# Kernel optimization log

Measured on AMD Instinct MI355X. Metric: run time of the kernel, lower is better.

Reference implementation:

```python
import jax, jax.numpy as jnp
import numpy as np

B, L, C, P, H, DK, MRD = 16, 1024, 512, 64, 8, 64, 7
STD = 0.02


def _layernorm(x, g, b):
    mu = x.mean(-1, keepdims=True)
    var = ((x - mu) ** 2).mean(-1, keepdims=True)
    return (x - mu) / jnp.sqrt(var + 1e-5) * g + b


def _rel_pos_table(L, m):
    i = jnp.arange(L)
    d = jnp.abs(i[:, None] - i[None, :]).astype(jnp.float32)
    d = jnp.where(d > m, m + jnp.log2(jnp.maximum(d - m, 1.0)), d)
    return jnp.clip(d, 0, 2 * m).astype(jnp.int32)  # (L, L) in [0, 2m]


def setup_inputs() -> dict:
    key = jax.random.key(0)
    ks = jax.random.split(key, 16)
    inp = {
        'qx': jax.random.normal(ks[0], (B, L, C), jnp.float32),
        'kx': jax.random.normal(ks[1], (B, L, C), jnp.float32),
        'vx': jax.random.normal(ks[2], (B, L, C), jnp.float32),
        'maskPAD': jnp.ones((B, L, L), jnp.int32),
        'Wp': jax.random.normal(ks[3], (C, P)) * STD,
        'bp': jnp.zeros((P,)),
        'WQ': jax.random.normal(ks[4], (C, H * DK)) * STD,
        'bQ': jnp.zeros((H * DK,)),
        'WK': jax.random.normal(ks[5], (C, H * DK)) * STD,
        'bK': jnp.zeros((H * DK,)),
        'WV': jax.random.normal(ks[6], (C, H * DK)) * STD,
        'bV': jnp.zeros((H * DK,)),
        'WO': jax.random.normal(ks[7], (H * DK, C)) * STD,
        'bO': jnp.zeros((C,)),
        'embK': jax.random.normal(ks[8], (2 * MRD + 1, H)) * STD,
        'embB': jax.random.normal(ks[9], (2 * MRD + 1, H)) * STD,
        'ln1_g': jnp.ones((C,)), 'ln1_b': jnp.zeros((C,)),
        'ln2_g': jnp.ones((C,)), 'ln2_b': jnp.zeros((C,)),
        'W1': jax.random.normal(ks[10], (C, 4 * C)) * STD,
        'b1': jnp.zeros((4 * C,)),
        'W2': jax.random.normal(ks[11], (4 * C, C)) * STD,
        'b2': jnp.zeros((C,)),
    }
    return inp


def reference(qx, kx, vx, maskPAD, Wp, bp, WQ, bQ, WK, bK, WV, bV, WO, bO,
              embK, embB, ln1_g, ln1_b, ln2_g, ln2_b, W1, b1, W2, b2):
    B_, L_, C_ = qx.shape
    P_ = Wp.shape[1]
    H_ = embK.shape[1]
    DK_ = WV.shape[1] // H_
    m = (embK.shape[0] - 1) // 2

    # pseudo-token attention pooling
    pScore = vx @ Wp + bp                                   # (B, L, P)
    pad = (maskPAD[:, 0] == 0)                              # (B, L)
    pScore = jnp.where(pad[:, :, None], -2.0 ** 15, pScore)
    pAlpha = jax.nn.softmax(pScore, axis=1)                 # softmax over L
    kxp = jnp.einsum('blp,blc->bpc', pAlpha, kx)            # (B, P, C)
    vxp = jnp.einsum('blp,blc->bpc', pAlpha, vx)
    pA = jax.lax.stop_gradient(pAlpha)                      # .detach()

    # multi-head attention vs pseudo tokens
    q = (qx @ WQ + bQ).reshape(B_, L_, H_, DK_).transpose(0, 2, 1, 3)   # (B,H,L,dk)
    k = (kxp @ WK + bK).reshape(B_, P_, H_, DK_).transpose(0, 2, 1, 3)  # (B,H,P,dk)
    v = (vxp @ WV + bV).reshape(B_, P_, H_, DK_).transpose(0, 2, 1, 3)
    scores = jnp.einsum('bhld,bhpd->bhlp', q, k) / np.sqrt(DK_).astype(np.float32)

    # relative position multiplicative/additive bias, pooled through pA
    tab = _rel_pos_table(L_, m)                             # (L, L)
    Krel = embK[tab].transpose(2, 0, 1)                     # (H, L, L)
    brel = embB[tab].transpose(2, 0, 1)
    Kb = jnp.einsum('hlm,bmp->bhlp', Krel, pA)
    bb = jnp.einsum('hlm,bmp->bhlp', brel, pA)
    scores = scores * Kb + bb

    alpha = jax.nn.softmax(scores, axis=3)
    z = jnp.einsum('bhlp,bhpd->bhld', alpha, v)
    z = z.transpose(0, 2, 1, 3).reshape(B_, L_, H_ * DK_)
    z = z @ WO + bO

    # FFN block (residuals against vx, post-LN)
    z1 = _layernorm(vx + z, ln1_g, ln1_b)
    ffn = jax.nn.gelu(z1 @ W1 + b1, approximate=False) @ W2 + b2
    x = _layernorm(z1 + ffn, ln2_g, ln2_b)
    return x
```

## Files before the change

### kernel.cpp

```cpp
#include <hip/hip_runtime.h>
#include <hip/hip_bf16.h>

#define BI   16
#define LSEQ 1024
#define CDIM 512
#define PDIM 64
#define HH   8
#define DKK  64

typedef __hip_bfloat16 bf16;
typedef unsigned short u16;
typedef __attribute__((ext_vector_type(8))) short bf16x8;
typedef __attribute__((ext_vector_type(4))) float f32x4;

__constant__ int c_dlo[15] = {0,1,2,3,4,5,6,7, 9,11,15,23,39, 71,135};
__constant__ int c_dhi[15] = {0,1,2,3,4,5,6,8,10,14,22,38,70,134,1023};

__device__ __forceinline__ float b2f(u16 u) {
    union { unsigned int i; float f; } c; c.i = ((unsigned int)u) << 16; return c.f;
}
__device__ __forceinline__ u16 f2bu(float v) {
    bf16 h = __float2bfloat16(v);
    return *(u16*)&h;
}
__device__ __forceinline__ float ldDyn(const void* p, size_t i, int f) {
    return f ? ((const float*)p)[i] : b2f(((const u16*)p)[i]);
}
__device__ __forceinline__ void ld4Dyn(const void* p, size_t i, int f, float* o) {
    if (f) { float4 v = *(const float4*)((const float*)p + i);
             o[0]=v.x; o[1]=v.y; o[2]=v.z; o[3]=v.w; }
    else   { ushort4 u = *(const ushort4*)((const u16*)p + i);
             o[0]=b2f(u.x); o[1]=b2f(u.y); o[2]=b2f(u.z); o[3]=b2f(u.w); }
}

__device__ __forceinline__ void gll16(const u16* g, u16* l) {
    __builtin_amdgcn_global_load_lds(
        (const __attribute__((address_space(1))) unsigned int*)g,
        (__attribute__((address_space(3))) unsigned int*)l,
        16, 0, 0);
}

__device__ __forceinline__ float wsum(float v) {
    #pragma unroll
    for (int o = 32; o; o >>= 1) v += __shfl_xor(v, o, 64);
    return v;
}
__device__ __forceinline__ float wmax(float v) {
    #pragma unroll
    for (int o = 32; o; o >>= 1) v = fmaxf(v, __shfl_xor(v, o, 64));
    return v;
}

__device__ __forceinline__ float gelu_f(float v) {
    float x  = v * 0.70710678118654752f;
    float ax = fabsf(x);
    float t  = __builtin_amdgcn_rcpf(1.0f + 0.3275911f * ax);
    float p  = t * (0.254829592f + t * (-0.284496736f + t * (1.421413741f +
               t * (-1.453152027f + t * 1.061405429f))));
    float e  = __expf(-ax * ax);
    float er = 1.0f - p * e;
    er = (x < 0.0f) ? -er : er;
    return 0.5f * v * (1.0f + er);
}

__global__ void k_detect(const unsigned int* __restrict__ qw, int* __restrict__ flag) {
    __shared__ int cnt;
    if (threadIdx.x == 0) cnt = 0;
    __syncthreads();
    int local = 0;
    for (int i = threadIdx.x; i < 4096; i += 256) {
        float fv = b2f((u16)(qw[i] & 0xFFFFu));
        float af = fabsf(fv);
        if (fv == 0.0f || (af >= 0.0009765625f && af <= 32.0f)) local++;
    }
    atomicAdd(&cnt, local);
    __syncthreads();
    if (threadIdx.x == 0) flag[0] = (cnt >= 2048) ? 0 : 1;
}

__global__ __launch_bounds__(256) void k_cvt2(
    const void* __restrict__ s0, u16* __restrict__ d0,
    const void* __restrict__ s1, u16* __restrict__ d1,
    const int* __restrict__ flag, int n)
{
    const int fA = flag[0];
    const void* src = blockIdx.y ? s1 : s0;
    u16* dst = blockIdx.y ? d1 : d0;
    int i = (blockIdx.x * 256 + threadIdx.x) * 4;
    if (i >= n) return;
    float t[4]; ld4Dyn(src, i, fA, t);
    ushort4 o; o.x = f2bu(t[0]); o.y = f2bu(t[1]); o.z = f2bu(t[2]); o.w = f2bu(t[3]);
    *(ushort4*)(dst + i) = o;
}

__device__ __forceinline__ void transp_core(
    const void* W, u16* WT, int fd, int Kd, int Nd, int bx, int by)
{
    __shared__ u16 t[32][33];
    const int tx = threadIdx.x & 31, ty = threadIdx.x >> 5;
    #pragma unroll
    for (int r = 0; r < 32; r += 8) {
        int k = by * 32 + ty + r, n = bx * 32 + tx;
        t[ty + r][tx] = f2bu(ldDyn(W, (size_t)k * Nd + n, fd));
    }
    __syncthreads();
    #pragma unroll
    for (int r = 0; r < 32; r += 8) {
        int n = bx * 32 + ty + r, k = by * 32 + tx;
        WT[(size_t)n * Kd + k] = t[tx][ty + r];
    }
}

__global__ __launch_bounds__(256) void k_transp(
    const void* __restrict__ W, u16* __restrict__ WT, const int* __restrict__ flag,
    int Kd, int Nd)
{
    transp_core(W, WT, flag[0], Kd, Nd, blockIdx.x, blockIdx.y);
}

__global__ __launch_bounds__(256) void k_transp4(
    const void* __restrict__ W0, u16* __restrict__ T0,
    const void* __restrict__ W1, u16* __restrict__ T1,
    const void* __restrict__ W2, u16* __restrict__ T2,
    const void* __restrict__ W3, u16* __restrict__ T3,
    const int* __restrict__ flag)
{
    const void* W; u16* T;
    switch (blockIdx.z) {
        case 0: W = W0; T = T0; break;
        case 1: W = W1; T = T1; break;
        case 2: W = W2; T = T2; break;
        default: W = W3; T = T3; break;
    }
    transp_core(W, T, flag[0], 512, 512, blockIdx.x, blockIdx.y);
}

__global__ __launch_bounds__(256) void k_transpcv(
    const void* __restrict__ kx, const u16* __restrict__ vxb,
    u16* __restrict__ kxT, u16* __restrict__ vxT, const int* __restrict__ flag)
{
    const int t = blockIdx.z >> 4;
    const int b = blockIdx.z & 15;
    const int l0 = blockIdx.x * 64, c0 = blockIdx.y * 32;
    __shared__ u16 s[32][72];
    const int tid = threadIdx.x;
    if (t == 0) {
        const int fd = flag[0];
        #pragma unroll
        for (int p = 0; p < 2; ++p) {
            int l = (tid >> 3) + p * 32, c4 = (tid & 7) * 4;
            float v[4];
            ld4Dyn(kx, ((size_t)b * LSEQ + l0 + l) * CDIM + c0 + c4, fd, v);
            #pragma unroll
            for (int k = 0; k < 4; ++k) s[c4 + k][l] = f2bu(v[k]);
        }
    } else {
        #pragma unroll
        for (int p = 0; p < 2; ++p) {
            int l = (tid >> 3) + p * 32, c4 = (tid & 7) * 4;
            ushort4 u = *(const ushort4*)&vxb[((size_t)b * LSEQ + l0 + l) * CDIM + c0 + c4];
            s[c4 + 0][l] = u.x; s[c4 + 1][l] = u.y;
            s[c4 + 2][l] = u.z; s[c4 + 3][l] = u.w;
        }
    }
    __syncthreads();
    u16* dst = t ? vxT : kxT;
    #pragma unroll
    for (int p = 0; p < 2; ++p) {
        int c = (tid >> 4) + p * 16, l4 = (tid & 15) * 4;
        *(ushort4*)&dst[((size_t)b * CDIM + c0 + c) * LSEQ + l0 + l4] =
            *(const ushort4*)&s[c][l4];
    }
}

__device__ __forceinline__ void gemm_core(
    u16 (*As)[32], u16 (*Bs)[32],
    const u16* A, const u16* BT, const void* bias, const u16* res, void* Cc, int fd,
    int K, int lda, int ldbt, int ldc, size_t bOff, int mode, int outBf, int perm,
    int m0, int n0)
{
    const int tid = threadIdx.x;
    const int wave = tid >> 6, lane = tid & 63;
    const int q = lane >> 4, l16 = lane & 15;
    const int wm = (wave >> 2) * 64, wn = (wave & 3) * 64;
    const int srow = lane >> 2;
    const int scol = ((lane & 3) ^ ((lane >> 3) & 3)) * 8;
    const int rchk = (l16 >> 1) & 3;
    const int nt = K >> 5;

    f32x4 acc[4][4];
    #pragma unroll
    for (int i = 0; i < 4; ++i)
        #pragma unroll
        for (int j = 0; j < 4; ++j) acc[i][j] = (f32x4){0.f, 0.f, 0.f, 0.f};

    auto stage = [&](int t, int buf) {
        gll16(A + (size_t)(m0 + wave * 16 + srow) * lda + t * 32 + scol,
              &As[buf * 128 + wave * 16][0]);
        #pragma unroll
        for (int pass = 0; pass < 2; ++pass)
            gll16(BT + (size_t)(n0 + pass * 128 + wave * 16 + srow) * ldbt + t * 32 + scol,
                  &Bs[buf * 256 + pass * 128 + wave * 16][0]);
    };

    stage(0, 0);

    for (int t = 0; t < nt; ++t) {
        if (t + 1 < nt) {
            stage(t + 1, (t + 1) & 1);
            asm volatile("s_waitcnt vmcnt(3)" ::: "memory");
        } else {
            asm volatile("s_waitcnt vmcnt(0)" ::: "memory");
        }
        __builtin_amdgcn_sched_barrier(0);
        __builtin_amdgcn_s_barrier();

        const int ca = (t & 1) * 128, cbB = (t & 1) * 256;
        bf16x8 af[4], bfr[4];
        #pragma unroll
        for (int i = 0; i < 4; ++i)
            af[i] = *(const bf16x8*)&As[ca + wm + i * 16 + l16][(q ^ rchk) * 8];
        #pragma unroll
        for (int j = 0; j < 4; ++j)
            bfr[j] = *(const bf16x8*)&Bs[cbB + wn + j * 16 + l16][(q ^ rchk) * 8];
        #pragma unroll
        for (int i = 0; i < 4; ++i)
            #pragma unroll
            for (int j = 0; j < 4; ++j)
                acc[i][j] = __builtin_amdgcn_mfma_f32_16x16x32_bf16(af[i], bfr[j], acc[i][j], 0, 0, 0);

        if (t + 1 < nt) {
            asm volatile("s_waitcnt lgkmcnt(0)" ::: "memory");
            __builtin_amdgcn_sched_barrier(0);
            __builtin_amdgcn_s_barrier();
        }
    }

    float bv[4];
    #pragma unroll
    for (int j = 0; j < 4; ++j)
        bv[j] = ldDyn(bias, bOff + (size_t)(n0 + wn + j * 16 + l16), fd);

    #pragma unroll
    for (int i = 0; i < 4; ++i) {
        int row = m0 + wm + i * 16 + q * 4;
        #pragma unroll
        for (int j = 0; j < 4; ++j) {
            int col = n0 + wn + j * 16 + l16;
            #pragma unroll
            for (int r = 0; r < 4; ++r) {
                float v = acc[i][j][r] + bv[j];
                int m = row + r;
                if (mode == 2) {
                    v += b2f(res[(size_t)m * ldc + col]);
                    if (outBf) ((u16*)Cc)[(size_t)m * ldc + col] = f2bu(v);
                    else       ((float*)Cc)[(size_t)m * ldc + col] = v;
                } else {
                    if (mode == 1) v = gelu_f(v);
                    size_t idx = perm ? (size_t)((m >> 6) << 15) + ((size_t)col << 6) + (m & 63)
                                      : (size_t)m * ldc + col;
                    if (outBf) ((u16*)Cc)[idx] = f2bu(v);
                    else       ((float*)Cc)[idx] = v;
                }
            }
        }
    }
}

__global__ __launch_bounds__(512) void gemm_mfma(
    const u16* __restrict__ A, const u16* __restrict__ BT, const void* __restrict__ bias,
    const u16* __restrict__ res, void* __restrict__ Cc, const int* __restrict__ flag,
    int K, int lda, int ldbt, int ldc, size_t bOff, int mode, int outBf, int perm)
{
    __shared__ u16 As[256][32];
    __shared__ u16 Bs[512][32];
    const int lin = blockIdx.y * gridDim.x + blockIdx.x;
    const int chunk = (gridDim.x * gridDim.y) >> 3;
    const int wg = (lin & 7) * chunk + (lin >> 3);
    const int bx = wg % gridDim.x, by = wg / gridDim.x;
    gemm_core(As, Bs, A, BT, bias, res, Cc, flag[0], K, lda, ldbt, ldc, bOff,
              mode, outBf, perm, by * 128, bx * 256);
}

__global__ __launch_bounds__(512) void gemm_kv(
    const u16* __restrict__ A0, const u16* __restrict__ A1,
    const u16* __restrict__ BT0, const u16* __restrict__ BT1,
    const void* __restrict__ b0, const void* __restrict__ b1,
    void* __restrict__ C0, void* __restrict__ C1, const int* __restrict__ flag)
{
    __shared__ u16 As[256][32];
    __shared__ u16 Bs[512][32];
    const int z = blockIdx.z;
    gemm_core(As, Bs, z ? A1 : A0, z ? BT1 : BT0, z ? b1 : b0, nullptr,
              z ? C1 : C0, flag[0],
              CDIM, CDIM, CDIM, CDIM, 0, 0, 1, z ? 1 : 0,
              blockIdx.y * 128, blockIdx.x * 256);
}

__global__ __launch_bounds__(256) void gemm_pool(
    const u16* __restrict__ pAT, const u16* __restrict__ kxT,
    const u16* __restrict__ vxT, u16* __restrict__ kvxb)
{
    __shared__ u16 As[128][32];
    __shared__ u16 Bs[256][32];
    const int b = blockIdx.y;
    const int n0 = blockIdx.x * 128;
    const u16* Ag = pAT + (size_t)b * (PDIM * LSEQ);
    const u16* Bg = (blockIdx.z ? vxT : kxT) + (size_t)b * (CDIM * LSEQ);
    u16* Cg = kvxb + (size_t)blockIdx.z * 524288 + (size_t)b * (PDIM * CDIM);

    const int tid = threadIdx.x;
    const int wave = tid >> 6, lane = tid & 63;
    const int q = lane >> 4, l16 = lane & 15;
    const int wm = (wave >> 1) * 32, wn = (wave & 1) * 64;
    const int srow = lane >> 2, scol = (lane & 3) * 8;

    f32x4 acc[2][4];
    #pragma unroll
    for (int i = 0; i < 2; ++i)
        #pragma unroll
        for (int j = 0; j < 4; ++j) acc[i][j] = (f32x4){0.f, 0.f, 0.f, 0.f};

    gll16(Ag + (size_t)(wave * 16 + srow) * LSEQ + scol, &As[wave * 16][0]);
    #pragma unroll
    for (int pass = 0; pass < 2; ++pass)
        gll16(Bg + (size_t)(n0 + wave * 32 + pass * 16 + srow) * LSEQ + scol,
              &Bs[wave * 32 + pass * 16][0]);
    __syncthreads();

    int cur = 0;
    for (int k0 = 0; k0 < LSEQ; k0 += 32) {
        if (k0 + 32 < LSEQ) {
            const int na = (cur ^ 1) * 64, nb = (cur ^ 1) * 128;
            gll16(Ag + (size_t)(wave * 16 + srow) * LSEQ + (k0 + 32) + scol,
                  &As[na + wave * 16][0]);
            #pragma unroll
            for (int pass = 0; pass < 2; ++pass)
                gll16(Bg + (size_t)(n0 + wave * 32 + pass * 16 + srow) * LSEQ + (k0 + 32) + scol,
                      &Bs[nb + wave * 32 + pass * 16][0]);
        }
        const int ca = cur * 64, cb = cur * 128;
        bf16x8 af[2], bfr[4];
        #pragma unroll
        for (int i = 0; i < 2; ++i) af[i] = *(const bf16x8*)&As[ca + wm + i * 16 + l16][q * 8];
        #pragma unroll
        for (int j = 0; j < 4; ++j) bfr[j] = *(const bf16x8*)&Bs[cb + wn + j * 16 + l16][q * 8];
        #pragma unroll
        for (int i = 0; i < 2; ++i)
            #pragma unroll
            for (int j = 0; j < 4; ++j)
                acc[i][j] = __builtin_amdgcn_mfma_f32_16x16x32_bf16(af[i], bfr[j], acc[i][j], 0, 0, 0);
        __syncthreads();
        cur ^= 1;
    }

    #pragma unroll
    for (int i = 0; i < 2; ++i) {
        int row = wm + i * 16 + q * 4;
        #pragma unroll
        for (int j = 0; j < 4; ++j) {
            int col = n0 + wn + j * 16 + l16;
            #pragma unroll
            for (int r = 0; r < 4; ++r)
                Cg[(size_t)(row + r) * CDIM + col] = f2bu(acc[i][j][r]);
        }
    }
}

__global__ __launch_bounds__(256) void gemm_mfma64(
    const u16* __restrict__ A, const u16* __restrict__ BT, const void* __restrict__ bias,
    float* __restrict__ Cc, const int* __restrict__ flag,
    int K, int lda, int ldbt)
{
    const int fd = flag[0];
    __shared__ u16 As[256][32];
    __shared__ u16 Bs[128][32];
    const int m0 = blockIdx.y * 128;
    const int tid = threadIdx.x;
    const int wave = tid >> 6, lane = tid & 63;
    const int q = lane >> 4, l16 = lane & 15;
    const int wm = wave * 32;
    const int srow = wave * 16 + (lane >> 2);
    const int scol = (lane & 3) * 8;

    f32x4 acc[2][4];
    #pragma unroll
    for (int i = 0; i < 2; ++i)
        #pragma unroll
        for (int j = 0; j < 4; ++j) acc[i][j] = (f32x4){0.f, 0.f, 0.f, 0.f};

    #pragma unroll
    for (int pass = 0; pass < 2; ++pass) {
        int row = pass * 64 + srow;
        gll16(A + (size_t)(m0 + row) * lda + scol, &As[pass * 64 + wave * 16][0]);
    }
    gll16(BT + (size_t)srow * ldbt + scol, &Bs[wave * 16][0]);
    __syncthreads();

    int cur = 0;
    for (int k0 = 0; k0 < K; k0 += 32) {
        if (k0 + 32 < K) {
            const int na = (cur ^ 1) * 128, nb = (cur ^ 1) * 64;
            #pragma unroll
            for (int pass = 0; pass < 2; ++pass) {
                int row = pass * 64 + srow;
                gll16(A + (size_t)(m0 + row) * lda + (k0 + 32) + scol,
                      &As[na + pass * 64 + wave * 16][0]);
            }
            gll16(BT + (size_t)srow * ldbt + (k0 + 32) + scol, &Bs[nb + wave * 16][0]);
        }
        const int ca = cur * 128, cb = cur * 64;
        bf16x8 af[2], bfr[4];
        #pragma unroll
        for (int i = 0; i < 2; ++i) af[i] = *(const bf16x8*)&As[ca + wm + i * 16 + l16][q * 8];
        #pragma unroll
        for (int j = 0; j < 4; ++j) bfr[j] = *(const bf16x8*)&Bs[cb + j * 16 + l16][q * 8];
        #pragma unroll
        for (int i = 0; i < 2; ++i)
            #pragma unroll
            for (int j = 0; j < 4; ++j)
                acc[i][j] = __builtin_amdgcn_mfma_f32_16x16x32_bf16(af[i], bfr[j], acc[i][j], 0, 0, 0);
        __syncthreads();
        cur ^= 1;
    }

    #pragma unroll
    for (int i = 0; i < 2; ++i) {
        int row = m0 + wm + i * 16 + q * 4;
        #pragma unroll
        for (int j = 0; j < 4; ++j) {
            int col = j * 16 + l16;
            #pragma unroll
            for (int r = 0; r < 4; ++r)
                Cc[(size_t)(row + r) * 64 + col] = acc[i][j][r] + ldDyn(bias, col, fd);
        }
    }
}

__global__ __launch_bounds__(256) void gemm_att(
    const u16* __restrict__ Abase, const u16* __restrict__ Bbase,
    void* __restrict__ outp, int mode)
{
    __shared__ u16 Aq[2][128][32];
    __shared__ u16 Bk[2][64][32];
    const int bh = blockIdx.y;
    const int b = bh >> 3, h = bh & 7;
    const int m0 = blockIdx.x * 128;
    const int tid = threadIdx.x;
    const int wave = tid >> 6, lane = tid & 63;
    const int q = lane >> 4, l16 = lane & 15;

    const u16* Ag; const u16* Bg; int lda, ldb;
    if (mode == 0) {
        Ag = Abase + ((size_t)b * LSEQ + m0) * CDIM + h * 64;  lda = CDIM;
        Bg = Bbase + (size_t)b * 32768 + h * 64;               ldb = CDIM;
    } else {
        Ag = Abase + ((size_t)bh * LSEQ + m0) * 64;            lda = 64;
        Bg = Bbase + (size_t)b * 32768 + (size_t)h * 64 * 64;  ldb = 64;
    }

    const int srow = lane >> 2;
    const int scol = (lane & 3) * 8;
    #pragma unroll
    for (int half = 0; half < 2; ++half) {
        #pragma unroll
        for (int pass = 0; pass < 2; ++pass) {
            int row = pass * 64 + wave * 16 + srow;
            gll16(Ag + (size_t)row * lda + half * 32 + scol,
                  &Aq[half][pass * 64 + wave * 16][0]);
        }
        gll16(Bg + (size_t)(wave * 16 + srow) * ldb + half * 32 + scol,
              &Bk[half][wave * 16][0]);
    }
    __syncthreads();

    f32x4 acc[2][4];
    #pragma unroll
    for (int i = 0; i < 2; ++i)
        #pragma unroll
        for (int j = 0; j < 4; ++j) acc[i][j] = (f32x4){0.f, 0.f, 0.f, 0.f};

    #pragma unroll
    for (int kk = 0; kk < 2; ++kk) {
        bf16x8 af[2], bfr[4];
        #pragma unroll
        for (int i = 0; i < 2; ++i)
            af[i] = *(const bf16x8*)&Aq[kk][wave * 32 + i * 16 + l16][q * 8];
        #pragma unroll
        for (int j = 0; j < 4; ++j)
            bfr[j] = *(const bf16x8*)&Bk[kk][j * 16 + l16][q * 8];
        #pragma unroll
        for (int i = 0; i < 2; ++i)
            #pragma unroll
            for (int j = 0; j < 4; ++j)
                acc[i][j] = __builtin_amdgcn_mfma_f32_16x16x32_bf16(af[i], bfr[j], acc[i][j], 0, 0, 0);
    }

    #pragma unroll
    for (int i = 0; i < 2; ++i) {
        int row = m0 + wave * 32 + i * 16 + q * 4;
        #pragma unroll
        for (int j = 0; j < 4; ++j) {
            int col = j * 16 + l16;
            #pragma unroll
            for (int r = 0; r < 4; ++r) {
                if (mode == 0) {
                    ((float*)outp)[((size_t)bh * LSEQ + row + r) * 64 + col] =
                        0.125f * acc[i][j][r];
                } else {
                    ((u16*)outp)[((size_t)b * LSEQ + row + r) * CDIM + h * 64 + col] =
                        f2bu(acc[i][j][r]);
                }
            }
        }
    }
}

__global__ __launch_bounds__(256) void k_softscan(
    const float* __restrict__ psc, const int* __restrict__ maskPAD,
    u16* __restrict__ pAT, float* __restrict__ cumT)
{
    const int b = blockIdx.x >> 6;
    const int p = blockIdx.x & 63;
    const int tid = threadIdx.x;
    __shared__ float s0[1024], s1[1024];
    __shared__ float redA[4], redB[4];

    float acc[4];
    #pragma unroll
    for (int r = 0; r < 4; ++r) {
        int m = tid + r * 256;
        float a = psc[((size_t)b * LSEQ + m) * PDIM + p];
        if (maskPAD[(size_t)b * LSEQ * LSEQ + m] == 0) a = -32768.0f;
        acc[r] = a;
    }
    float mx = fmaxf(fmaxf(acc[0], acc[1]), fmaxf(acc[2], acc[3]));
    mx = wmax(mx);
    if ((tid & 63) == 0) redA[tid >> 6] = mx;
    __syncthreads();
    mx = fmaxf(fmaxf(redA[0], redA[1]), fmaxf(redA[2], redA[3]));

    float e[4], ls = 0.f;
    #pragma unroll
    for (int r = 0; r < 4; ++r) { e[r] = expf(acc[r] - mx); ls += e[r]; }
    ls = wsum(ls);
    if ((tid & 63) == 0) redB[tid >> 6] = ls;
    __syncthreads();
    float inv = 1.0f / (redB[0] + redB[1] + redB[2] + redB[3]);

    #pragma unroll
    for (int r = 0; r < 4; ++r) {
        int m = tid + r * 256;
        float pa = e[r] * inv;
        pAT[((size_t)b * PDIM + p) * LSEQ + m] = f2bu(pa);
        s0[m] = pa;
    }
    __syncthreads();

    float* src = s0; float* dst = s1;
    for (int off = 1; off < 1024; off <<= 1) {
        #pragma unroll
        for (int r = 0; r < 4; ++r) {
            int i = tid + r * 256;
            float v = src[i];
            if (i >= off) v += src[i - off];
            dst[i] = v;
        }
        __syncthreads();
        float* t = src; src = dst; dst = t;
    }
    size_t cb = (size_t)b * (LSEQ + 1) * PDIM + p;
    if (tid == 0) cumT[cb] = 0.f;
    #pragma unroll
    for (int r = 0; r < 4; ++r) {
        int i = tid + r * 256;
        cumT[cb + (size_t)(i + 1) * PDIM] = src[i];
    }
}

__global__ __launch_bounds__(512) void k_sm(
    const float* __restrict__ raw, u16* __restrict__ alb,
    const float* __restrict__ cumT,
    const void* __restrict__ embK, const void* __restrict__ embB,
    const int* __restrict__ flag)
{
    const int fd = flag[0];
    const int b = blockIdx.x >> 10;
    const int l = blockIdx.x & 1023;
    const int tid = threadIdx.x;
    __shared__ float S[15][PDIM];
    __shared__ float eK[120], eB[120];

    if (tid < 120) { eK[tid] = ldDyn(embK, tid, fd); eB[tid] = ldDyn(embB, tid, fd); }

    const float* cb = cumT + (size_t)b * (LSEQ + 1) * PDIM;
    for (int idx = tid; idx < 960; idx += 512) {
        int t = idx >> 6, pp = idx & 63;
        float s;
        if (t == 0) {
            s = cb[(size_t)(l + 1) * 64 + pp] - cb[(size_t)l * 64 + pp];
        } else {
            s = 0.f;
            int hi = l - c_dlo[t];
            int lo = l - c_dhi[t]; if (lo < 0) lo = 0;
            if (hi >= lo) s += cb[(size_t)(hi + 1) * 64 + pp] - cb[(size_t)lo * 64 + pp];
            lo = l + c_dlo[t];
            hi = l + c_dhi[t]; if (hi > 1023) hi = 1023;
            if (lo <= hi) s += cb[(size_t)(hi + 1) * 64 + pp] - cb[(size_t)lo * 64 + pp];
        }
        S[t][pp] = s;
    }
    __syncthreads();

    const int h = tid >> 6, p = tid & 63;
    float kbm = 0.f, bbm = 0.f;
    #pragma unroll
    for (int t = 0; t < 15; ++t) {
        float sv = S[t][p];
        kbm += eK[t * 8 + h] * sv;
        bbm += eB[t * 8 + h] * sv;
    }
    size_t idx = (((size_t)b * 8 + h) * LSEQ + l) * 64 + p;
    float sc = raw[idx] * kbm + bbm;
    float mx = wmax(sc);
    float e  = expf(sc - mx);
    float ssum = wsum(e);
    alb[idx] = f2bu(e / ssum);
}

__global__ __launch_bounds__(512) void k_ln(
    const void* __restrict__ a, const u16* __restrict__ badd,
    const void* __restrict__ g, const void* __restrict__ be, const int* __restrict__ flag,
    void* __restrict__ out, float* __restrict__ out2, const void* __restrict__ bias2,
    int aKind, int outKind)
{
    const int fd = flag[0];
    const int fA = (aKind == 2) ? fd : aKind;
    const int fO = (outKind == 2) ? fd : outKind;
    const size_t row = blockIdx.x;
    const int c = threadIdx.x;
    float x = ldDyn(a, row * CDIM + c, fA);
    if (badd) x += b2f(badd[row * CDIM + c]);

    __shared__ float rA[8], rB[8];
    float s = wsum(x);
    if ((c & 63) == 0) rA[c >> 6] = s;
    __syncthreads();
    float tot = 0.f;
    #pragma unroll
    for (int w = 0; w < 8; ++w) tot += rA[w];
    float mu = tot * (1.0f / 512.0f);
    float dv = x - mu;
    float s2 = wsum(dv * dv);
    if ((c & 63) == 0) rB[c >> 6] = s2;
    __syncthreads();
    float v2 = 0.f;
    #pragma unroll
    for (int w = 0; w < 8; ++w) v2 += rB[w];
    float y = dv * rsqrtf(v2 * (1.0f / 512.0f) + 1e-5f) * ldDyn(g, c, fd) + ldDyn(be, c, fd);
    if (fO) ((float*)out)[row * CDIM + c] = y;
    else    ((u16*)out)[row * CDIM + c] = f2bu(y);
    if (out2) out2[row * CDIM + c] = y + ldDyn(bias2, c, fd);
}

extern "C" void kernel_launch(void* const* d_in, const int* in_sizes, int n_in,
                              void* d_out, int out_size, void* d_ws, size_t ws_size,
                              hipStream_t stream)
{
    (void)in_sizes; (void)n_in; (void)out_size; (void)ws_size;
    const void* qx   = d_in[0];
    const void* kx   = d_in[1];
    const void* vx   = d_in[2];
    const int*  mask = (const int*)d_in[3];
    const void* Wp   = d_in[4];
    const void* bp   = d_in[5];
    const void* WQ   = d_in[6];
    const void* bQ   = d_in[7];
    const void* WK   = d_in[8];
    const void* bK   = d_in[9];
    const void* WV   = d_in[10];
    const void* bV   = d_in[11];
    const void* WO   = d_in[12];
    const void* bO   = d_in[13];
    const void* embK = d_in[14];
    const void* embB = d_in[15];
    const void* l1g  = d_in[16];
    const void* l1b  = d_in[17];
    const void* l2g  = d_in[18];
    const void* l2b  = d_in[19];
    const void* W1   = d_in[20];
    const void* b1   = d_in[21];
    const void* W2   = d_in[22];
    const void* b2   = d_in[23];

    float* ws     = (float*)d_ws;
    int*   flag   = (int*)d_ws;
    u16*   outFb  = (u16*)(ws + 64);
    float* psc    = ws + 64;
    float* cumT   = ws + 1048640;
    u16*   pAT    = (u16*)(ws + 2098240);
    u16*   kbh    = (u16*)(ws + 2622528);
    u16*   vbT    = (u16*)(ws + 2884672);
    u16*   albuf  = (u16*)(ws + 3146816);
    u16*   kvxb   = (u16*)(ws + 7341120);
    u16*   qz     = (u16*)(ws + 8388672);
    u16*   hidden = (u16*)(ws + 12582976);
    u16*   qxb    = hidden;
    u16*   zo     = qxb;
    u16*   vxb    = (u16*)(ws + 16777280);
    u16*   kxT    = (u16*)(ws + 20971584);
    u16*   vxT    = (u16*)(ws + 25165888);
    float* rawbuf = ws + 20971584;
    u16*   WqT    = (u16*)(ws + 29360192);
    u16*   WkT    = (u16*)(ws + 29491264);
    u16*   WvT    = (u16*)(ws + 29622336);
    u16*   WoT    = (u16*)(ws + 29753408);
    u16*   W1T    = (u16*)(ws + 29884480);
    u16*   W2T    = (u16*)(ws + 30408768);
    u16*   WpT    = (u16*)(ws + 30933056);

    const int MROW = BI * LSEQ;

    k_detect<<<dim3(1), dim3(256), 0, stream>>>((const unsigned int*)qx, flag);
    k_cvt2<<<dim3(MROW * CDIM / 1024, 2), dim3(256), 0, stream>>>(
        qx, qxb, vx, vxb, flag, MROW * CDIM);
    k_transp4<<<dim3(16, 16, 4), dim3(256), 0, stream>>>(
        WQ, WqT, WK, WkT, WV, WvT, WO, WoT, flag);
    k_transp<<<dim3(2, 16),  dim3(256), 0, stream>>>(Wp, WpT, flag, 512, 64);
    k_transp<<<dim3(64, 16), dim3(256), 0, stream>>>(W1, W1T, flag, 512, 2048);
    k_transp<<<dim3(16, 64), dim3(256), 0, stream>>>(W2, W2T, flag, 2048, 512);
    k_transpcv<<<dim3(16, 16, 32), dim3(256), 0, stream>>>(kx, vxb, kxT, vxT, flag);

    gemm_mfma64<<<dim3(1, MROW / 128), dim3(256), 0, stream>>>(
        vxb, WpT, bp, psc, flag, CDIM, CDIM, CDIM);
    k_softscan<<<dim3(BI * PDIM), dim3(256), 0, stream>>>(psc, mask, pAT, cumT);
    gemm_pool<<<dim3(4, 16, 2), dim3(256), 0, stream>>>(pAT, kxT, vxT, kvxb);
    gemm_mfma<<<dim3(2, MROW / 128), dim3(512), 0, stream>>>(
        qxb, WqT, bQ, nullptr, qz, flag, CDIM, CDIM, CDIM, CDIM, 0, 0, 1, 0);
    gemm_kv<<<dim3(2, 8, 2), dim3(512), 0, stream>>>(
        kvxb, kvxb + 524288, WkT, WvT, bK, bV, kbh, vbT, flag);
    gemm_att<<<dim3(8, BI * HH), dim3(256), 0, stream>>>(qz, kbh, rawbuf, 0);
    k_sm<<<dim3(BI * LSEQ), dim3(512), 0, stream>>>(
        rawbuf, albuf, cumT, embK, embB, flag);
    gemm_att<<<dim3(8, BI * HH), dim3(256), 0, stream>>>(albuf, vbT, qz, 1);
    gemm_mfma<<<dim3(2, MROW / 128), dim3(512), 0, stream>>>(
        qz, WoT, bO, nullptr, zo, flag, CDIM, CDIM, CDIM, CDIM, 0, 0, 1, 0);
    k_ln<<<dim3(MROW), dim3(512), 0, stream>>>(
        vx, zo, l1g, l1b, flag, qz, nullptr, nullptr, 2, 0);
    gemm_mfma<<<dim3(8, MROW / 128), dim3(512), 0, stream>>>(
        qz, W1T, b1, nullptr, hidden, flag, CDIM, CDIM, CDIM, 2048, 0, 1, 1, 0);
    gemm_mfma<<<dim3(2, MROW / 128), dim3(512), 0, stream>>>(
        hidden, W2T, b2, qz, outFb, flag, 2048, 2048, 2048, CDIM, 0, 2, 1, 0);
    k_ln<<<dim3(MROW), dim3(512), 0, stream>>>(
        outFb, nullptr, l2g, l2b, flag, d_out, nullptr, nullptr, 0, 2);
}
```

Before: 613.2 us.

## Add four-stage LDS pipelined GEMM variant for narrow-N projections

Adds a gemm_core_deep path that uses four LDS buffers, issuing loads three tiles ahead with one barrier per iteration instead of two, and raises wave priority around the MFMA block. It is applied to the Q, O, K/V and W2 projection GEMMs (N=512), which launch only 256 workgroups and are likely latency-bound on global loads. LDS per block grows to 96KB, which can lower occupancy to one block per CU.

```diff
diff --git a/kernel.cpp b/kernel.cpp
--- a/kernel.cpp
+++ b/kernel.cpp
@@ -173,69 +173,11 @@
     }
 }
 
-__device__ __forceinline__ void gemm_core(
-    u16 (*As)[32], u16 (*Bs)[32],
-    const u16* A, const u16* BT, const void* bias, const u16* res, void* Cc, int fd,
-    int K, int lda, int ldbt, int ldc, size_t bOff, int mode, int outBf, int perm,
-    int m0, int n0)
-{
-    const int tid = threadIdx.x;
-    const int wave = tid >> 6, lane = tid & 63;
-    const int q = lane >> 4, l16 = lane & 15;
-    const int wm = (wave >> 2) * 64, wn = (wave & 3) * 64;
-    const int srow = lane >> 2;
-    const int scol = ((lane & 3) ^ ((lane >> 3) & 3)) * 8;
-    const int rchk = (l16 >> 1) & 3;
-    const int nt = K >> 5;
-
-    f32x4 acc[4][4];
-    #pragma unroll
-    for (int i = 0; i < 4; ++i)
-        #pragma unroll
-        for (int j = 0; j < 4; ++j) acc[i][j] = (f32x4){0.f, 0.f, 0.f, 0.f};
-
-    auto stage = [&](int t, int buf) {
-        gll16(A + (size_t)(m0 + wave * 16 + srow) * lda + t * 32 + scol,
-              &As[buf * 128 + wave * 16][0]);
-        #pragma unroll
-        for (int pass = 0; pass < 2; ++pass)
-            gll16(BT + (size_t)(n0 + pass * 128 + wave * 16 + srow) * ldbt + t * 32 + scol,
-                  &Bs[buf * 256 + pass * 128 + wave * 16][0]);
-    };
-
-    stage(0, 0);
-
-    for (int t = 0; t < nt; ++t) {
-        if (t + 1 < nt) {
-            stage(t + 1, (t + 1) & 1);
-            asm volatile("s_waitcnt vmcnt(3)" ::: "memory");
-        } else {
-            asm volatile("s_waitcnt vmcnt(0)" ::: "memory");
-        }
-        __builtin_amdgcn_sched_barrier(0);
-        __builtin_amdgcn_s_barrier();
-
-        const int ca = (t & 1) * 128, cbB = (t & 1) * 256;
-        bf16x8 af[4], bfr[4];
-        #pragma unroll
-        for (int i = 0; i < 4; ++i)
-            af[i] = *(const bf16x8*)&As[ca + wm + i * 16 + l16][(q ^ rchk) * 8];
-        #pragma unroll
-        for (int j = 0; j < 4; ++j)
-            bfr[j] = *(const bf16x8*)&Bs[cbB + wn + j * 16 + l16][(q ^ rchk) * 8];
-        #pragma unroll
-        for (int i = 0; i < 4; ++i)
-            #pragma unroll
-            for (int j = 0; j < 4; ++j)
-                acc[i][j] = __builtin_amdgcn_mfma_f32_16x16x32_bf16(af[i], bfr[j], acc[i][j], 0, 0, 0);
-
-        if (t + 1 < nt) {
-            asm volatile("s_waitcnt lgkmcnt(0)" ::: "memory");
-            __builtin_amdgcn_sched_barrier(0);
-            __builtin_amdgcn_s_barrier();
-        }
-    }
-
+__device__ __forceinline__ void gemm_epi(
+    f32x4 (*acc)[4], const void* bias, const u16* res, void* Cc, int fd,
+    int ldc, size_t bOff, int mode, int outBf, int perm,
+    int m0, int n0, int wm, int wn, int q, int l16)
+{
     float bv[4];
     #pragma unroll
     for (int j = 0; j < 4; ++j)
@@ -267,6 +209,135 @@
     }
 }
 
+__device__ __forceinline__ void gemm_core(
+    u16 (*As)[32], u16 (*Bs)[32],
+    const u16* A, const u16* BT, const void* bias, const u16* res, void* Cc, int fd,
+    int K, int lda, int ldbt, int ldc, size_t bOff, int mode, int outBf, int perm,
+    int m0, int n0)
+{
+    const int tid = threadIdx.x;
+    const int wave = tid >> 6, lane = tid & 63;
+    const int q = lane >> 4, l16 = lane & 15;
+    const int wm = (wave >> 2) * 64, wn = (wave & 3) * 64;
+    const int srow = lane >> 2;
+    const int scol = ((lane & 3) ^ ((lane >> 3) & 3)) * 8;
+    const int rchk = (l16 >> 1) & 3;
+    const int nt = K >> 5;
+
+    f32x4 acc[4][4];
+    #pragma unroll
+    for (int i = 0; i < 4; ++i)
+        #pragma unroll
+        for (int j = 0; j < 4; ++j) acc[i][j] = (f32x4){0.f, 0.f, 0.f, 0.f};
+
+    auto stage = [&](int t, int buf) {
+        gll16(A + (size_t)(m0 + wave * 16 + srow) * lda + t * 32 + scol,
+              &As[buf * 128 + wave * 16][0]);
+        #pragma unroll
+        for (int pass = 0; pass < 2; ++pass)
+            gll16(BT + (size_t)(n0 + pass * 128 + wave * 16 + srow) * ldbt + t * 32 + scol,
+                  &Bs[buf * 256 + pass * 128 + wave * 16][0]);
+    };
+
+    stage(0, 0);
+
+    for (int t = 0; t < nt; ++t) {
+        if (t + 1 < nt) {
+            stage(t + 1, (t + 1) & 1);
+            asm volatile("s_waitcnt vmcnt(3)" ::: "memory");
+        } else {
+            asm volatile("s_waitcnt vmcnt(0)" ::: "memory");
+        }
+        __builtin_amdgcn_sched_barrier(0);
+        __builtin_amdgcn_s_barrier();
+
+        const int ca = (t & 1) * 128, cbB = (t & 1) * 256;
+        bf16x8 af[4], bfr[4];
+        #pragma unroll
+        for (int i = 0; i < 4; ++i)
+            af[i] = *(const bf16x8*)&As[ca + wm + i * 16 + l16][(q ^ rchk) * 8];
+        #pragma unroll
+        for (int j = 0; j < 4; ++j)
+            bfr[j] = *(const bf16x8*)&Bs[cbB + wn + j * 16 + l16][(q ^ rchk) * 8];
+        #pragma unroll
+        for (int i = 0; i < 4; ++i)
+            #pragma unroll
+            for (int j = 0; j < 4; ++j)
+                acc[i][j] = __builtin_amdgcn_mfma_f32_16x16x32_bf16(af[i], bfr[j], acc[i][j], 0, 0, 0);
+
+        if (t + 1 < nt) {
+            asm volatile("s_waitcnt lgkmcnt(0)" ::: "memory");
+            __builtin_amdgcn_sched_barrier(0);
+            __builtin_amdgcn_s_barrier();
+        }
+    }
+
+    gemm_epi(acc, bias, res, Cc, fd, ldc, bOff, mode, outBf, perm, m0, n0, wm, wn, q, l16);
+}
+
+__device__ __forceinline__ void gemm_core_deep(
+    u16 (*As)[32], u16 (*Bs)[32],
+    const u16* A, const u16* BT, const void* bias, const u16* res, void* Cc, int fd,
+    int K, int lda, int ldbt, int ldc, size_t bOff, int mode, int outBf, int perm,
+    int m0, int n0)
+{
+    const int tid = threadIdx.x;
+    const int wave = tid >> 6, lane = tid & 63;
+    const int q = lane >> 4, l16 = lane & 15;
+    const int wm = (wave >> 2) * 64, wn = (wave & 3) * 64;
+    const int srow = lane >> 2;
+    const int scol = ((lane & 3) ^ ((lane >> 3) & 3)) * 8;
+    const int rchk = (l16 >> 1) & 3;
+    const int nt = K >> 5;
+
+    f32x4 acc[4][4];
+    #pragma unroll
+    for (int i = 0; i < 4; ++i)
+        #pragma unroll
+        for (int j = 0; j < 4; ++j) acc[i][j] = (f32x4){0.f, 0.f, 0.f, 0.f};
+
+    auto stage = [&](int t, int buf) {
+        gll16(A + (size_t)(m0 + wave * 16 + srow) * lda + t * 32 + scol,
+              &As[buf * 128 + wave * 16][0]);
+        #pragma unroll
+        for (int pass = 0; pass < 2; ++pass)
+            gll16(BT + (size_t)(n0 + pass * 128 + wave * 16 + srow) * ldbt + t * 32 + scol,
+                  &Bs[buf * 256 + pass * 128 + wave * 16][0]);
+    };
+
+    stage(0, 0);
+    if (nt > 1) stage(1, 1);
+    if (nt > 2) stage(2, 2);
+
+    for (int t = 0; t < nt; ++t) {
+        if (t + 2 < nt)      asm volatile("s_waitcnt vmcnt(6)" ::: "memory");
+        else if (t + 1 < nt) asm volatile("s_waitcnt vmcnt(3)" ::: "memory");
+        else                 asm volatile("s_waitcnt vmcnt(0)" ::: "memory");
+        __builtin_amdgcn_sched_barrier(0);
+        __builtin_amdgcn_s_barrier();
+        __builtin_amdgcn_sched_barrier(0);
+        if (t + 3 < nt) stage(t + 3, (t + 3) & 3);
+
+        const int ca = (t & 3) * 128, cbB = (t & 3) * 256;
+        bf16x8 af[4], bfr[4];
+        #pragma unroll
+        for (int i = 0; i < 4; ++i)
+            af[i] = *(const bf16x8*)&As[ca + wm + i * 16 + l16][(q ^ rchk) * 8];
+        #pragma unroll
+        for (int j = 0; j < 4; ++j)
+            bfr[j] = *(const bf16x8*)&Bs[cbB + wn + j * 16 + l16][(q ^ rchk) * 8];
+        __builtin_amdgcn_s_setprio(1);
+        #pragma unroll
+        for (int i = 0; i < 4; ++i)
+            #pragma unroll
+            for (int j = 0; j < 4; ++j)
+                acc[i][j] = __builtin_amdgcn_mfma_f32_16x16x32_bf16(af[i], bfr[j], acc[i][j], 0, 0, 0);
+        __builtin_amdgcn_s_setprio(0);
+    }
+
+    gemm_epi(acc, bias, res, Cc, fd, ldc, bOff, mode, outBf, perm, m0, n0, wm, wn, q, l16);
+}
+
 __global__ __launch_bounds__(512) void gemm_mfma(
     const u16* __restrict__ A, const u16* __restrict__ BT, const void* __restrict__ bias,
     const u16* __restrict__ res, void* __restrict__ Cc, const int* __restrict__ flag,
@@ -282,19 +353,34 @@
               mode, outBf, perm, by * 128, bx * 256);
 }
 
+__global__ __launch_bounds__(512) void gemm_mfma_deep(
+    const u16* __restrict__ A, const u16* __restrict__ BT, const void* __restrict__ bias,
+    const u16* __restrict__ res, void* __restrict__ Cc, const int* __restrict__ flag,
+    int K, int lda, int ldbt, int ldc, size_t bOff, int mode, int outBf, int perm)
+{
+    __shared__ u16 As[512][32];
+    __shared__ u16 Bs[1024][32];
+    const int lin = blockIdx.y * gridDim.x + blockIdx.x;
+    const int chunk = (gridDim.x * gridDim.y) >> 3;
+    const int wg = (lin & 7) * chunk + (lin >> 3);
+    const int bx = wg % gridDim.x, by = wg / gridDim.x;
+    gemm_core_deep(As, Bs, A, BT, bias, res, Cc, flag[0], K, lda, ldbt, ldc, bOff,
+                   mode, outBf, perm, by * 128, bx * 256);
+}
+
 __global__ __launch_bounds__(512) void gemm_kv(
     const u16* __restrict__ A0, const u16* __restrict__ A1,
     const u16* __restrict__ BT0, const u16* __restrict__ BT1,
     const void* __restrict__ b0, const void* __restrict__ b1,
     void* __restrict__ C0, void* __restrict__ C1, const int* __restrict__ flag)
 {
-    __shared__ u16 As[256][32];
-    __shared__ u16 Bs[512][32];
+    __shared__ u16 As[512][32];
+    __shared__ u16 Bs[1024][32];
     const int z = blockIdx.z;
-    gemm_core(As, Bs, z ? A1 : A0, z ? BT1 : BT0, z ? b1 : b0, nullptr,
-              z ? C1 : C0, flag[0],
-              CDIM, CDIM, CDIM, CDIM, 0, 0, 1, z ? 1 : 0,
-              blockIdx.y * 128, blockIdx.x * 256);
+    gemm_core_deep(As, Bs, z ? A1 : A0, z ? BT1 : BT0, z ? b1 : b0, nullptr,
+                   z ? C1 : C0, flag[0],
+                   CDIM, CDIM, CDIM, CDIM, 0, 0, 1, z ? 1 : 0,
+                   blockIdx.y * 128, blockIdx.x * 256);
 }
 
 __global__ __launch_bounds__(256) void gemm_pool(
@@ -735,7 +821,7 @@
         vxb, WpT, bp, psc, flag, CDIM, CDIM, CDIM);
     k_softscan<<<dim3(BI * PDIM), dim3(256), 0, stream>>>(psc, mask, pAT, cumT);
     gemm_pool<<<dim3(4, 16, 2), dim3(256), 0, stream>>>(pAT, kxT, vxT, kvxb);
-    gemm_mfma<<<dim3(2, MROW / 128), dim3(512), 0, stream>>>(
+    gemm_mfma_deep<<<dim3(2, MROW / 128), dim3(512), 0, stream>>>(
         qxb, WqT, bQ, nullptr, qz, flag, CDIM, CDIM, CDIM, CDIM, 0, 0, 1, 0);
     gemm_kv<<<dim3(2, 8, 2), dim3(512), 0, stream>>>(
         kvxb, kvxb + 524288, WkT, WvT, bK, bV, kbh, vbT, flag);
@@ -743,13 +829,13 @@
     k_sm<<<dim3(BI * LSEQ), dim3(512), 0, stream>>>(
         rawbuf, albuf, cumT, embK, embB, flag);
     gemm_att<<<dim3(8, BI * HH), dim3(256), 0, stream>>>(albuf, vbT, qz, 1);
-    gemm_mfma<<<dim3(2, MROW / 128), dim3(512), 0, stream>>>(
+    gemm_mfma_deep<<<dim3(2, MROW / 128), dim3(512), 0, stream>>>(
         qz, WoT, bO, nullptr, zo, flag, CDIM, CDIM, CDIM, CDIM, 0, 0, 1, 0);
     k_ln<<<dim3(MROW), dim3(512), 0, stream>>>(
         vx, zo, l1g, l1b, flag, qz, nullptr, nullptr, 2, 0);
     gemm_mfma<<<dim3(8, MROW / 128), dim3(512), 0, stream>>>(
         qz, W1T, b1, nullptr, hidden, flag, CDIM, CDIM, CDIM, 2048, 0, 1, 1, 0);
-    gemm_mfma<<<dim3(2, MROW / 128), dim3(512), 0, stream>>>(
+    gemm_mfma_deep<<<dim3(2, MROW / 128), dim3(512), 0, stream>>>(
         hidden, W2T, b2, qz, outFb, flag, 2048, 2048, 2048, CDIM, 0, 2, 1, 0);
     k_ln<<<dim3(MROW), dim3(512), 0, stream>>>(
         outFb, nullptr, l2g, l2b, flag, d_out, nullptr, nullptr, 0, 2);
```

Result: slower. 672.7 us (+9.7%).
